# Optimization experiments

Measured on AMD Instinct MI355X. Metric: run time of the kernel, lower is better.

The kernel has to match this reference:

```python
import jax, jax.numpy as jnp
import numpy as np

H = 512          # hidden_size
HALF = 256       # hidden_size // 2 (RGCN feature dim)
NHEAD = 8
NLAYER = 12
NBLOCK = 2
NENT = 50000
NREL = 12
NBASES = 8
NEDGE = 500000
TXTD = 768       # raw text/image feature dim
BATCH, ELEN, SLEN = 32, 50, 128


def setup_inputs() -> dict:
    key = jax.random.key(0)
    ks = jax.random.split(key, 40)
    def p(i, shape, scale=0.02):
        return jax.random.normal(ks[i], shape, jnp.float32) * scale
    inp = {
        'entity_ids': jax.random.randint(ks[0], (BATCH, ELEN), 0, NENT),
        'token_embeds': jax.random.normal(ks[1], (BATCH, SLEN, H), jnp.float32),
        'edge_index': jax.random.randint(ks[2], (2, NEDGE), 0, NENT),
        'edge_type': jax.random.randint(ks[3], (NEDGE,), 0, NREL),
        'node_embeds': p(4, (NENT, HALF)),
        'rgcn_basis': p(5, (NBASES, HALF, HALF)),
        'rgcn_comp': p(6, (NREL, NBASES), 0.3),
        'rgcn_root': p(7, (HALF, HALF)),
        'rgcn_bias': p(8, (HALF,)),
        'kg_proj_w': p(9, (HALF, H)), 'kg_proj_b': p(10, (H,)),
        'text_proj_w': p(11, (TXTD, H)), 'text_proj_b': p(12, (H,)),
        'image_proj_w': p(13, (TXTD, H)), 'image_proj_b': p(14, (H,)),
        'cq_w': p(15, (H, H)), 'cq_b': p(16, (H,)),
        'kgk_w': p(17, (H, H)), 'kgk_b': p(18, (H,)),
        'imk_w': p(19, (H, H)), 'imk_b': p(20, (H,)),
        'txk_w': p(21, (H, H)), 'txk_b': p(22, (H,)),
        'pp1_w1': p(23, (H, HALF)), 'pp1_b1': p(24, (HALF,)),
        'pp1_w2': p(25, (HALF, H)), 'pp1_b2': p(26, (H,)),
        'pp2_w': p(27, (H, NLAYER * NBLOCK * H)), 'pp2_b': p(28, (NLAYER * NBLOCK * H,)),
        'text_embeds_init': p(29, (NENT, TXTD), 1.0),
        'image_embeds_init': p(30, (NENT, TXTD), 1.0),
    }
    return inp


def _rgcn(x, edge_index, edge_type, basis, comp, root, bias):
    # PyG RGCNConv with basis decomposition, aggr='mean', root weight + bias.
    # mean_{e: rel=r, dst=i}(x[src_e] @ W_r) == (mean_{e}(x[src_e])) @ W_r, so we
    # aggregate raw features per (dst, relation) segment then apply W_r once per node.
    N = x.shape[0]
    src, dst = edge_index[0], edge_index[1]
    seg = dst * NREL + edge_type                      # combined (node, relation) key
    msgs = x[src]                                     # [E, HALF] gather
    agg = jax.ops.segment_sum(msgs, seg, num_segments=N * NREL)
    cnt = jax.ops.segment_sum(jnp.ones((src.shape[0],), x.dtype), seg, num_segments=N * NREL)
    mean = (agg / jnp.maximum(cnt, 1.0)[:, None]).reshape(N, NREL, HALF)
    w_rel = jnp.einsum('rb,bio->rio', comp, basis)    # [R, HALF, HALF]
    out = jnp.einsum('nri,rio->no', mean, w_rel) + x @ root + bias
    return out


def reference(entity_ids, token_embeds, edge_index, edge_type, node_embeds,
              rgcn_basis, rgcn_comp, rgcn_root, rgcn_bias,
              kg_proj_w, kg_proj_b, text_proj_w, text_proj_b,
              image_proj_w, image_proj_b, cq_w, cq_b,
              kgk_w, kgk_b, imk_w, imk_b, txk_w, txk_b,
              pp1_w1, pp1_b1, pp1_w2, pp1_b2, pp2_w, pp2_b,
              text_embeds_init, image_embeds_init):
    kg_all = _rgcn(node_embeds, edge_index, edge_type, rgcn_basis, rgcn_comp, rgcn_root, rgcn_bias)
    kg_all = kg_all @ kg_proj_w + kg_proj_b           # [N, H]
    kg_feat = kg_all[entity_ids]                      # [B, L, H]
    text_feat = text_embeds_init[entity_ids] @ text_proj_w + text_proj_b
    image_feat = image_embeds_init[entity_ids] @ image_proj_w + image_proj_b
    # context-guided fusion
    q = (jnp.mean(token_embeds, axis=1) @ cq_w + cq_b)[:, None, :]   # [B, 1, H]
    kg_s = jnp.sum(q * (kg_feat @ kgk_w + kgk_b), -1, keepdims=True)
    img_s = jnp.sum(q * (image_feat @ imk_w + imk_b), -1, keepdims=True)
    txt_s = jnp.sum(q * (text_feat @ txk_w + txk_b), -1, keepdims=True)
    w = jax.nn.softmax(jnp.concatenate([kg_s, img_s, txt_s], axis=-1), axis=-1)
    fused = w[..., 0:1] * kg_feat + w[..., 1:2] * image_feat + w[..., 2:3] * text_feat
    # prompt expansion
    h = jax.nn.relu(fused @ pp1_w1 + pp1_b1) @ pp1_w2 + pp1_b2 + fused
    p = h @ pp2_w + pp2_b                             # [B, L, NLAYER*NBLOCK*H]
    B, L = entity_ids.shape
    p = p.reshape(B, L, NLAYER, NBLOCK, NHEAD, H // NHEAD)
    p = jnp.transpose(p, (2, 3, 0, 4, 1, 5))          # [layer, block, B, head, L, head_dim]
    loss_cl = jnp.float32(0.0)                        # output_entity=False path
    return p, loss_cl
```

## Files before the change

### kernel.cpp

```cpp
#include <hip/hip_runtime.h>

#define HDIM 512
#define HALF 256
#define NRELS 12
#define NBASES 8
#define NLAYERS 12
#define NBLOCKS 2
#define NHEADS 8
#define NENTS 50000
#define TXTD 768
#define BATCH 32
#define ELEN 50
#define SLEN 128
#define NPOS (BATCH * ELEN)
#define NSEG (NPOS * NRELS)
#define BCAP 64

typedef unsigned short u16;
typedef __attribute__((ext_vector_type(8))) __bf16 bf16x8;
typedef __attribute__((ext_vector_type(4))) float f32x4;

__device__ __forceinline__ u16 f2bf(float f) {
    unsigned int u = __float_as_uint(f);
    unsigned int r = (u + 0x7FFFu + ((u >> 16) & 1u)) >> 16;
    return (u16)r;
}
__device__ __forceinline__ float bf2f(u16 v) {
    return __uint_as_float(((unsigned int)v) << 16);
}

#define ASYNC_COPY16(g, l)                                                              \
    __builtin_amdgcn_global_load_lds((const __attribute__((address_space(1))) void*)(g), \
                                     (__attribute__((address_space(3))) unsigned int*)(l), 16, 0, 0)

__global__ void init_kernel(int* __restrict__ map, int* __restrict__ segcnt,
                            int* __restrict__ nuniq, float* __restrict__ zb,
                            const float* __restrict__ kgb, const float* __restrict__ imb,
                            const float* __restrict__ txb, u16* __restrict__ SW,
                            const float* __restrict__ rgcn_bias,
                            const float* __restrict__ kg_proj_w,
                            const float* __restrict__ kg_proj_b,
                            float* __restrict__ biasC, float* __restrict__ out_last) {
    int blk = blockIdx.x;
    int t = threadIdx.x;
    if (blk >= 128) {
        int n = (blk - 128) * 256 + t;
        float acc = kg_proj_b[n];
        for (int c = 0; c < HALF; ++c) acc += rgcn_bias[c] * kg_proj_w[(size_t)c * HDIM + n];
        biasC[n] = acc;
        return;
    }
    int tid = blk * 256 + t;
    const int nt = 128 * 256;
    int4 m4 = {-1, -1, -1, -1};
    for (int i = tid; i < NENTS / 4; i += nt) ((int4*)map)[i] = m4;
    int4 z4 = {0, 0, 0, 0};
    for (int i = tid; i < NSEG / 4; i += nt) ((int4*)segcnt)[i] = z4;
    for (int i = tid; i < 2304; i += nt) zb[i] = 0.f;
    if (tid < HDIM) {
        SW[(size_t)1536 * HDIM + tid] = f2bf(kgb[tid]);
        SW[(size_t)1537 * HDIM + tid] = f2bf(imb[tid]);
        SW[(size_t)1538 * HDIM + tid] = f2bf(txb[tid]);
    }
    if (tid == 0) { *nuniq = 0; *out_last = 0.f; }
}

__global__ void dedup_kernel(const int* __restrict__ eid, int* __restrict__ map,
                             int* __restrict__ uniq, int* __restrict__ nuniq) {
    int i = blockIdx.x * blockDim.x + threadIdx.x;
    if (i >= NPOS) return;
    int n = eid[i];
    int old = atomicCAS(&map[n], -1, -2);
    if (old == -1) {
        int idx = atomicAdd(nuniq, 1);
        uniq[idx] = n;
        __threadfence();
        map[n] = idx;
    }
}

struct PrepArgs {
    const float* src[12];
    u16* dst[12];
};

__global__ __launch_bounds__(256) void midprep_kernel(
    const float* __restrict__ tok, u16* __restrict__ TMEAN,
    const int* __restrict__ uniq, const int* __restrict__ nuniq,
    const float* __restrict__ txi, const float* __restrict__ imi,
    u16* __restrict__ TXIN, u16* __restrict__ IMIN,
    const int* __restrict__ ei, const int* __restrict__ et, const int* __restrict__ map,
    int* __restrict__ segcnt, int* __restrict__ bucket, int E, PrepArgs a) {
    int blk = blockIdx.x;
    int t = threadIdx.x;
    if (blk < 64) {
        int b = blk >> 1;
        int col = (blk & 1) * 256 + t;
        float s = 0.f;
        for (int si = 0; si < SLEN; ++si) s += tok[((size_t)b * SLEN + si) * HDIM + col];
        TMEAN[(size_t)b * HDIM + col] = f2bf(s * (1.0f / SLEN));
    } else if (blk < 352) {
        if (t >= TXTD / 4) return;
        int nu = *nuniq;
        for (int u = blk - 64; u < NPOS; u += 288) {
            if (u >= nu) {
                ushort4 z = {0, 0, 0, 0};
                ((ushort4*)(TXIN + (size_t)u * TXTD))[t] = z;
                ((ushort4*)(IMIN + (size_t)u * TXTD))[t] = z;
                continue;
            }
            int n = uniq[u];
            float4 v = ((const float4*)(txi + (size_t)n * TXTD))[t];
            ushort4 o;
            o.x = f2bf(v.x); o.y = f2bf(v.y); o.z = f2bf(v.z); o.w = f2bf(v.w);
            ((ushort4*)(TXIN + (size_t)u * TXTD))[t] = o;
            v = ((const float4*)(imi + (size_t)n * TXTD))[t];
            o.x = f2bf(v.x); o.y = f2bf(v.y); o.z = f2bf(v.z); o.w = f2bf(v.w);
            ((ushort4*)(IMIN + (size_t)u * TXTD))[t] = o;
        }
    } else if (blk < 864) {
        const int* __restrict__ dstA = ei + E;
        int gtid = (blk - 352) * 256 + t;
        int e0 = gtid * 4;
        if (e0 + 3 < E) {
            int4 d4 = *(const int4*)(dstA + e0);
            int4 t4 = *(const int4*)(et + e0);
            int cc0 = map[d4.x], cc1 = map[d4.y], cc2 = map[d4.z], cc3 = map[d4.w];
            if (cc0 >= 0) {
                int seg = cc0 * NRELS + t4.x;
                int p = atomicAdd(&segcnt[seg], 1);
                if (p < BCAP) bucket[seg * BCAP + p] = ei[e0];
            }
            if (cc1 >= 0) {
                int seg = cc1 * NRELS + t4.y;
                int p = atomicAdd(&segcnt[seg], 1);
                if (p < BCAP) bucket[seg * BCAP + p] = ei[e0 + 1];
            }
            if (cc2 >= 0) {
                int seg = cc2 * NRELS + t4.z;
                int p = atomicAdd(&segcnt[seg], 1);
                if (p < BCAP) bucket[seg * BCAP + p] = ei[e0 + 2];
            }
            if (cc3 >= 0) {
                int seg = cc3 * NRELS + t4.w;
                int p = atomicAdd(&segcnt[seg], 1);
                if (p < BCAP) bucket[seg * BCAP + p] = ei[e0 + 3];
            }
        } else {
            for (int e = e0; e < E; ++e) {
                int c = map[dstA[e]];
                if (c >= 0) {
                    int seg = c * NRELS + et[e];
                    int p = atomicAdd(&segcnt[seg], 1);
                    if (p < BCAP) bucket[seg * BCAP + p] = ei[e];
                }
            }
        }
    } else {
        constexpr int NN[7]  = {512, 512, 512, 256, 512, 12288, 512};
        constexpr int LDT[7] = {256, 768, 768, 512, 256, 512, 512};
        constexpr int BASE[13] = {0, 32, 128, 224, 256, 288, 1824,
                                  1888, 2400, 2464, 2720, 2976, 3232};
        __shared__ u16 tb[64][65];
        int bid = blk - 864;
        int op = 0;
        #pragma unroll
        for (int i = 1; i < 12; ++i)
            if (bid >= BASE[i]) op = i;
        int idx = bid - BASE[op];
        if (op < 7) {
            int Nv = 0, ldt = 0;
            #pragma unroll
            for (int i = 0; i < 7; ++i)
                if (op == i) { Nv = NN[i]; ldt = LDT[i]; }
            int ncols = Nv >> 6;
            int n0 = (idx % ncols) * 64, k0 = (idx / ncols) * 64;
            const float* W = a.src[op];
            u16* WT = a.dst[op];
            int lane = t & 63, wv = t >> 6;
            #pragma unroll
            for (int i2 = 0; i2 < 16; ++i2) {
                int r = wv * 16 + i2;
                tb[r][lane] = f2bf(W[(size_t)(k0 + r) * Nv + n0 + lane]);
            }
            __syncthreads();
            #pragma unroll
            for (int i2 = 0; i2 < 16; ++i2) {
                int rr = wv * 16 + i2;
                WT[(size_t)(n0 + rr) * ldt + k0 + lane] = tb[lane][rr];
            }
        } else {
            int e = idx * 1024 + t * 4;
            float4 v = *(const float4*)(a.src[op] + e);
            ushort4 o;
            o.x = f2bf(v.x); o.y = f2bf(v.y); o.z = f2bf(v.z); o.w = f2bf(v.w);
            *(ushort4*)(a.dst[op] + e) = o;
        }
    }
}

template <int BM, int BN, int WM, int WN, bool SCATTER>
__device__ __forceinline__ void gemm_body(const u16* __restrict__ A, const u16* __restrict__ BT,
                                          const float* __restrict__ bias,
                                          void* __restrict__ Cout, int M, int N, int K,
                                          int bx, int by, bool outbf) {
    constexpr int MF = WM / 16, NF = WN / 16;
    constexpr int NWC = BN / WN;
    __shared__ u16 ldsA[BM][64];
    __shared__ u16 ldsB[BN][64];
    const int tid = threadIdx.x;
    const int lane = tid & 63;
    const int wv = tid >> 6;
    const int m0 = by * BM;
    const int n0 = bx * BN;
    const int wr = wv / NWC, wc = wv % NWC;
    const int srow = lane >> 3;
    const int sslot = lane & 7;

    f32x4 acc[MF][NF];
    #pragma unroll
    for (int i = 0; i < MF; ++i)
        #pragma unroll
        for (int j = 0; j < NF; ++j)
            #pragma unroll
            for (int r = 0; r < 4; ++r) acc[i][j][r] = 0.f;

    for (int k0 = 0; k0 < K; k0 += 64) {
        #pragma unroll
        for (int i = 0; i < BM / 32; ++i) {
            int R = wv * (BM / 4) + i * 8 + srow;
            int gm = m0 + R;
            gm = gm < M ? gm : M - 1;
            int s = sslot ^ (R & 7);
            ASYNC_COPY16(A + (size_t)gm * K + k0 + s * 8, &ldsA[wv * (BM / 4) + i * 8][0]);
        }
        #pragma unroll
        for (int i = 0; i < BN / 32; ++i) {
            int R = wv * (BN / 4) + i * 8 + srow;
            int s = sslot ^ (R & 7);
            ASYNC_COPY16(BT + (size_t)(n0 + R) * K + k0 + s * 8, &ldsB[wv * (BN / 4) + i * 8][0]);
        }
        __syncthreads();
        #pragma unroll
        for (int ks = 0; ks < 2; ++ks) {
            bf16x8 af[MF], bf[NF];
            int kg = ks * 4 + (lane >> 4);
            int rl = lane & 15;
            #pragma unroll
            for (int i = 0; i < MF; ++i) {
                int row = wr * WM + i * 16 + rl;
                af[i] = *(const bf16x8*)&ldsA[row][(kg ^ (row & 7)) * 8];
            }
            #pragma unroll
            for (int j = 0; j < NF; ++j) {
                int row = wc * WN + j * 16 + rl;
                bf[j] = *(const bf16x8*)&ldsB[row][(kg ^ (row & 7)) * 8];
            }
            #pragma unroll
            for (int i = 0; i < MF; ++i)
                #pragma unroll
                for (int j = 0; j < NF; ++j)
                    acc[i][j] = __builtin_amdgcn_mfma_f32_16x16x32_bf16(af[i], bf[j], acc[i][j], 0, 0, 0);
        }
        __syncthreads();
    }

    const int rl = lane & 15, rg = lane >> 4;
    #pragma unroll
    for (int i = 0; i < MF; ++i) {
        #pragma unroll
        for (int j = 0; j < NF; ++j) {
            int col = n0 + wc * WN + j * 16 + rl;
            float bv = bias[col];
            #pragma unroll
            for (int r = 0; r < 4; ++r) {
                int row = m0 + wr * WM + i * 16 + rg * 4 + r;
                if (row >= M) continue;
                float x = acc[i][j][r] + bv;
                if (SCATTER) {
                    int layer = col >> 10, blk = (col >> 9) & 1, head = (col >> 6) & 7, hd = col & 63;
                    int bb = row / ELEN, ll = row - bb * ELEN;
                    size_t oi = (((((size_t)layer * NBLOCKS + blk) * BATCH + bb) * NHEADS + head) * ELEN + ll) * 64 + hd;
                    ((float*)Cout)[oi] = x;
                } else if (outbf) {
                    ((u16*)Cout)[(size_t)row * N + col] = f2bf(x);
                } else {
                    ((float*)Cout)[(size_t)row * N + col] = x;
                }
            }
        }
    }
}

struct BuildArgs {
    const int *segcnt, *bucket, *uniq, *nuniq;
    const float *comp, *x;
    u16* MBX;
    const u16 *TMEAN, *CQT;
    const float* cq_b;
    u16* QB;
    const u16 *KGT, *W1f;
    const float* ZB;
    u16* WC;
    const u16 *TXIN, *TXT, *IMIN, *IMT;
    const float *txb, *imb;
    u16 *TXU, *IMU;
};
__global__ __launch_bounds__(256) void build_kernel(BuildArgs a) {
    int blk = blockIdx.x;
    if (blk >= NPOS) {
        const u16 *A, *BT;
        const float* bias;
        u16* C;
        int M, N, K, bx, by;
        if (blk >= NPOS + 8 + 288 + 200) {
            int i = blk - (NPOS + 8 + 288 + 200);
            A = a.IMIN; BT = a.IMT; bias = a.imb; C = a.IMU;
            M = NPOS; N = HDIM; K = TXTD; bx = i % 8; by = i / 8;
        } else if (blk >= NPOS + 8 + 288) {
            int i = blk - (NPOS + 8 + 288);
            A = a.TXIN; BT = a.TXT; bias = a.txb; C = a.TXU;
            M = NPOS; N = HDIM; K = TXTD; bx = i % 8; by = i / 8;
        } else if (blk >= NPOS + 8) {
            int i = blk - (NPOS + 8);
            A = a.KGT; BT = a.W1f; bias = a.ZB; C = a.WC;
            M = HDIM; N = 2304; K = HALF; bx = i % 36; by = i / 36;
        } else {
            A = a.TMEAN; BT = a.CQT; bias = a.cq_b; C = a.QB;
            M = BATCH; N = HDIM; K = HDIM; bx = blk - NPOS; by = 0;
        }
        gemm_body<64, 64, 32, 32, false>(A, BT, bias, C, M, N, K, bx, by, true);
        return;
    }
    int u = blk;
    int i = threadIdx.x;
    __shared__ float sc[NRELS * NBASES];
    if (i < NRELS * NBASES) sc[i] = a.comp[i];
    __syncthreads();
    u16* row = a.MBX + (size_t)u * 2304;
    int nu = *a.nuniq;
    if (u >= nu) {
        for (int b = 0; b < NBASES + 1; ++b) row[b * HALF + i] = 0;
        return;
    }
    float mr[NRELS];
    #pragma unroll
    for (int r = 0; r < NRELS; ++r) {
        int seg = u * NRELS + r;
        int c = a.segcnt[seg];
        int n = min(c, BCAP);
        float acc = 0.f;
        for (int e = 0; e < n; ++e) {
            int s = a.bucket[seg * BCAP + e];
            acc += a.x[(size_t)s * HALF + i];
        }
        mr[r] = acc * (1.f / fmaxf((float)c, 1.f));
    }
    #pragma unroll
    for (int b = 0; b < NBASES; ++b) {
        float v = 0.f;
        #pragma unroll
        for (int r = 0; r < NRELS; ++r) v += sc[r * NBASES + b] * mr[r];
        row[b * HALF + i] = f2bf(v);
    }
    row[NBASES * HALF + i] = f2bf(a.x[(size_t)a.uniq[u] * HALF + i]);
}

struct ProjArgs {
    const u16 *MBX, *WC, *QB, *SW;
    const float *biasC, *ZB;
    u16* KGU;
    float* QP;
};
__global__ __launch_bounds__(256) void proj_kernel(ProjArgs a) {
    int b = blockIdx.x;
    if (b < 200) {
        gemm_body<64, 64, 32, 32, false>(a.MBX, a.WC, a.biasC, a.KGU,
                                         NPOS, HDIM, 2304, b % 8, b / 8, true);
    } else {
        gemm_body<64, 64, 32, 32, false>(a.QB, a.SW, a.ZB, a.QP,
                                         BATCH, 1600, HDIM, b - 200, 0, false);
    }
}

__global__ __launch_bounds__(256) void tail_kernel(
    const int* __restrict__ eid, const int* __restrict__ map,
    const u16* __restrict__ KGU, const u16* __restrict__ IMU, const u16* __restrict__ TXU,
    const float* __restrict__ qp,
    const u16* __restrict__ W1T, const float* __restrict__ pp1_b1,
    const u16* __restrict__ W2T, const float* __restrict__ pp1_b2,
    u16* __restrict__ Hh) {
    __shared__ u16 FUS[16][520];
    __shared__ u16 P1s[16][264];
    const int bm0 = blockIdx.x * 16;
    const int lane = threadIdx.x & 63;
    const int wv = threadIdx.x >> 6;

    for (int rr = wv; rr < 16; rr += 4) {
        int bl = bm0 + rr;
        int b = bl / ELEN;
        int u = map[eid[bl]];
        const u16* kg = KGU + (size_t)u * HDIM;
        const u16* im = IMU + (size_t)u * HDIM;
        const u16* tx = TXU + (size_t)u * HDIM;
        const float* qrow = qp + (size_t)b * 1600;
        float pkg = 0.f, pim = 0.f, ptx = 0.f;
        for (int e = lane; e < HDIM; e += 64) {
            pkg += bf2f(kg[e]) * qrow[e];
            pim += bf2f(im[e]) * qrow[512 + e];
            ptx += bf2f(tx[e]) * qrow[1024 + e];
        }
        #pragma unroll
        for (int off = 32; off; off >>= 1) {
            pkg += __shfl_down(pkg, off);
            pim += __shfl_down(pim, off);
            ptx += __shfl_down(ptx, off);
        }
        float w0, w1, w2;
        if (lane == 0) {
            float av = pkg + qrow[1536];
            float c1 = pim + qrow[1537];
            float c2 = ptx + qrow[1538];
            float mx = fmaxf(av, fmaxf(c1, c2));
            float ea = __expf(av - mx), eb = __expf(c1 - mx), ec = __expf(c2 - mx);
            float inv = 1.f / (ea + eb + ec);
            w0 = ea * inv; w1 = eb * inv; w2 = ec * inv;
        }
        w0 = __shfl(w0, 0); w1 = __shfl(w1, 0); w2 = __shfl(w2, 0);
        for (int e = lane; e < HDIM; e += 64) {
            float v = w0 * bf2f(kg[e]) + w1 * bf2f(im[e]) + w2 * bf2f(tx[e]);
            FUS[rr][e] = f2bf(v);
        }
    }
    __syncthreads();

    {
        const int rl = lane & 15;
        const int kgrp = lane >> 4;
        f32x4 acc[4];
        #pragma unroll
        for (int j = 0; j < 4; ++j)
            #pragma unroll
            for (int r = 0; r < 4; ++r) acc[j][r] = 0.f;
        for (int kk = 0; kk < 512; kk += 32) {
            int k8 = kk + kgrp * 8;
            bf16x8 af = *(const bf16x8*)&FUS[rl][k8];
            bf16x8 bf[4];
            #pragma unroll
            for (int j = 0; j < 4; ++j) {
                int n = wv * 64 + j * 16 + rl;
                bf[j] = *(const bf16x8*)&W1T[(size_t)n * 512 + k8];
            }
            #pragma unroll
            for (int j = 0; j < 4; ++j)
                acc[j] = __builtin_amdgcn_mfma_f32_16x16x32_bf16(af, bf[j], acc[j], 0, 0, 0);
        }
        const int rg = lane >> 4;
        #pragma unroll
        for (int j = 0; j < 4; ++j) {
            int col = wv * 64 + j * 16 + rl;
            float bv = pp1_b1[col];
            #pragma unroll
            for (int r = 0; r < 4; ++r) {
                int row = rg * 4 + r;
                P1s[row][col] = f2bf(fmaxf(acc[j][r] + bv, 0.f));
            }
        }
    }
    __syncthreads();

    {
        const int rl = lane & 15;
        const int kgrp = lane >> 4;
        f32x4 acc[8];
        #pragma unroll
        for (int j = 0; j < 8; ++j)
            #pragma unroll
            for (int r = 0; r < 4; ++r) acc[j][r] = 0.f;
        for (int kk = 0; kk < 256; kk += 32) {
            int k8 = kk + kgrp * 8;
            bf16x8 af = *(const bf16x8*)&P1s[rl][k8];
            bf16x8 bf[8];
            #pragma unroll
            for (int j = 0; j < 8; ++j) {
                int n = wv * 128 + j * 16 + rl;
                bf[j] = *(const bf16x8*)&W2T[(size_t)n * 256 + k8];
            }
            #pragma unroll
            for (int j = 0; j < 8; ++j)
                acc[j] = __builtin_amdgcn_mfma_f32_16x16x32_bf16(af, bf[j], acc[j], 0, 0, 0);
        }
        const int rg = lane >> 4;
        #pragma unroll
        for (int j = 0; j < 8; ++j) {
            int col = wv * 128 + j * 16 + rl;
            float bv = pp1_b2[col];
            #pragma unroll
            for (int r = 0; r < 4; ++r) {
                int row = rg * 4 + r;
                float v = acc[j][r] + bv + bf2f(FUS[row][col]);
                Hh[(size_t)(bm0 + row) * HDIM + col] = f2bf(v);
            }
        }
    }
}

__global__ __launch_bounds__(256)
void pp2_kernel(const u16* __restrict__ A, const u16* __restrict__ BT,
                const float* __restrict__ bias, void* __restrict__ Cout,
                int M, int N, int K) {
    gemm_body<128, 128, 64, 64, true>(A, BT, bias, Cout, M, N, K, blockIdx.x, blockIdx.y, false);
}

extern "C" void kernel_launch(void* const* d_in, const int* in_sizes, int n_in,
                              void* d_out, int out_size, void* d_ws, size_t ws_size,
                              hipStream_t stream) {
    const int* entity_ids = (const int*)d_in[0];
    const float* token_embeds = (const float*)d_in[1];
    const int* edge_index = (const int*)d_in[2];
    const int* edge_type = (const int*)d_in[3];
    const float* node_embeds = (const float*)d_in[4];
    const float* rgcn_basis = (const float*)d_in[5];
    const float* rgcn_comp = (const float*)d_in[6];
    const float* rgcn_root = (const float*)d_in[7];
    const float* rgcn_bias = (const float*)d_in[8];
    const float* kg_proj_w = (const float*)d_in[9];
    const float* kg_proj_b = (const float*)d_in[10];
    const float* text_proj_w = (const float*)d_in[11];
    const float* text_proj_b = (const float*)d_in[12];
    const float* image_proj_w = (const float*)d_in[13];
    const float* image_proj_b = (const float*)d_in[14];
    const float* cq_w = (const float*)d_in[15];
    const float* cq_b = (const float*)d_in[16];
    const float* kgk_w = (const float*)d_in[17];
    const float* imk_w = (const float*)d_in[19];
    const float* txk_w = (const float*)d_in[21];
    const float* pp1_w1 = (const float*)d_in[23];
    const float* pp1_b1 = (const float*)d_in[24];
    const float* pp1_w2 = (const float*)d_in[25];
    const float* pp1_b2 = (const float*)d_in[26];
    const float* pp2_w = (const float*)d_in[27];
    const float* pp2_b = (const float*)d_in[28];
    const float* text_init = (const float*)d_in[29];
    const float* image_init = (const float*)d_in[30];

    const int E = in_sizes[3];

    size_t off = 0;
    auto alloc = [&](size_t bytes) { size_t o = off; off += (bytes + 255) & ~(size_t)255; return o; };
    char* ws = (char*)d_ws;
    size_t map_o  = alloc((size_t)NENTS * 4);
    size_t nun_o  = alloc(4);
    size_t unq_o  = alloc((size_t)NPOS * 4);
    size_t scnt_o = alloc((size_t)NSEG * 4);
    size_t bkt_o  = alloc((size_t)NSEG * BCAP * 4);
    size_t mbx_o  = alloc((size_t)NPOS * 2304 * 2);
    size_t w1f_o  = alloc((size_t)2304 * HALF * 2);
    size_t wc_o   = alloc((size_t)HDIM * 2304 * 2);
    size_t bc_o   = alloc((size_t)HDIM * 4);
    size_t kgt_o  = alloc((size_t)HDIM * HALF * 2);
    size_t kgu_o  = alloc((size_t)NPOS * HDIM * 2);
    size_t txin_o = alloc((size_t)NPOS * TXTD * 2);
    size_t imin_o = alloc((size_t)NPOS * TXTD * 2);
    size_t txt_o  = alloc((size_t)HDIM * TXTD * 2);
    size_t imt_o  = alloc((size_t)HDIM * TXTD * 2);
    size_t txu_o  = alloc((size_t)NPOS * HDIM * 2);
    size_t imu_o  = alloc((size_t)NPOS * HDIM * 2);
    size_t tm_o   = alloc((size_t)BATCH * HDIM * 2);
    size_t qb_o   = alloc((size_t)BATCH * HDIM * 2);
    size_t cqt_o  = alloc((size_t)HDIM * HDIM * 2);
    size_t sw_o   = alloc((size_t)1600 * HDIM * 2);
    size_t qp_o   = alloc((size_t)BATCH * 1600 * 4);
    size_t zb_o   = alloc((size_t)2304 * 4);
    size_t w1t_o  = alloc((size_t)HALF * HDIM * 2);
    size_t w2t_o  = alloc((size_t)HDIM * HALF * 2);
    size_t h_o    = alloc((size_t)NPOS * HDIM * 2);
    size_t pp2t_o = alloc((size_t)12288 * HDIM * 2);
    if (off > ws_size) return;

    int* map = (int*)(ws + map_o);
    int* nuniq = (int*)(ws + nun_o);
    int* uniq = (int*)(ws + unq_o);
    int* segcnt = (int*)(ws + scnt_o);
    int* bucket = (int*)(ws + bkt_o);
    u16* MBX = (u16*)(ws + mbx_o);
    u16* W1f = (u16*)(ws + w1f_o);
    u16* WC  = (u16*)(ws + wc_o);
    float* biasC = (float*)(ws + bc_o);
    u16* KGT = (u16*)(ws + kgt_o);
    u16* KGU = (u16*)(ws + kgu_o);
    u16* TXIN = (u16*)(ws + txin_o);
    u16* IMIN = (u16*)(ws + imin_o);
    u16* TXT = (u16*)(ws + txt_o);
    u16* IMT = (u16*)(ws + imt_o);
    u16* TXU = (u16*)(ws + txu_o);
    u16* IMU = (u16*)(ws + imu_o);
    u16* TMEAN = (u16*)(ws + tm_o);
    u16* QB  = (u16*)(ws + qb_o);
    u16* CQT = (u16*)(ws + cqt_o);
    u16* SW  = (u16*)(ws + sw_o);
    float* QP  = (float*)(ws + qp_o);
    float* ZB  = (float*)(ws + zb_o);
    u16* W1T = (u16*)(ws + w1t_o);
    u16* W2T = (u16*)(ws + w2t_o);
    u16* Hh  = (u16*)(ws + h_o);
    u16* PP2T = (u16*)(ws + pp2t_o);
    float* OUT = (float*)d_out;

    init_kernel<<<130, 256, 0, stream>>>(map, segcnt, nuniq, ZB,
                                         (const float*)d_in[18], (const float*)d_in[20],
                                         (const float*)d_in[22], SW,
                                         rgcn_bias, kg_proj_w, kg_proj_b, biasC,
                                         OUT + (out_size - 1));
    dedup_kernel<<<(NPOS + 255) / 256, 256, 0, stream>>>(entity_ids, map, uniq, nuniq);
    PrepArgs pa;
    pa.src[0] = kg_proj_w;    pa.dst[0] = KGT;
    pa.src[1] = text_proj_w;  pa.dst[1] = TXT;
    pa.src[2] = image_proj_w; pa.dst[2] = IMT;
    pa.src[3] = pp1_w1;       pa.dst[3] = W1T;
    pa.src[4] = pp1_w2;       pa.dst[4] = W2T;
    pa.src[5] = pp2_w;        pa.dst[5] = PP2T;
    pa.src[6] = cq_w;         pa.dst[6] = CQT;
    pa.src[7] = rgcn_basis;   pa.dst[7] = W1f;
    pa.src[8] = rgcn_root;    pa.dst[8] = W1f + (size_t)2048 * HALF;
    pa.src[9] = kgk_w;        pa.dst[9] = SW;
    pa.src[10] = imk_w;       pa.dst[10] = SW + (size_t)HDIM * HDIM;
    pa.src[11] = txk_w;       pa.dst[11] = SW + (size_t)2 * HDIM * HDIM;
    midprep_kernel<<<4096, 256, 0, stream>>>(token_embeds, TMEAN,
                                             uniq, nuniq, text_init, image_init, TXIN, IMIN,
                                             edge_index, edge_type, map, segcnt, bucket, E, pa);
    BuildArgs ba;
    ba.segcnt = segcnt; ba.bucket = bucket; ba.uniq = uniq; ba.nuniq = nuniq;
    ba.comp = rgcn_comp; ba.x = node_embeds; ba.MBX = MBX;
    ba.TMEAN = TMEAN; ba.CQT = CQT; ba.cq_b = cq_b; ba.QB = QB;
    ba.KGT = KGT; ba.W1f = W1f; ba.ZB = ZB; ba.WC = WC;
    ba.TXIN = TXIN; ba.TXT = TXT; ba.IMIN = IMIN; ba.IMT = IMT;
    ba.txb = text_proj_b; ba.imb = image_proj_b; ba.TXU = TXU; ba.IMU = IMU;
    build_kernel<<<NPOS + 8 + 288 + 400, 256, 0, stream>>>(ba);
    ProjArgs pr;
    pr.MBX = MBX; pr.WC = WC; pr.biasC = biasC; pr.KGU = KGU;
    pr.QB = QB; pr.SW = SW; pr.ZB = ZB; pr.QP = QP;
    proj_kernel<<<225, 256, 0, stream>>>(pr);
    tail_kernel<<<NPOS / 16, 256, 0, stream>>>(entity_ids, map, KGU, IMU, TXU, QP,
                                               W1T, pp1_b1, W2T, pp1_b2, Hh);
    pp2_kernel<<<dim3(12288 / 128, (NPOS + 127) / 128), 256, 0, stream>>>(
        Hh, PP2T, pp2_b, OUT, NPOS, 12288, HDIM);
}
```

Measured before the change: 152.3 us.

## Replace pp2 GEMM with dedicated 128x256 tile, 8-wave kernel with fused transpose store

The final large projection GEMM no longer uses the generic gemm_body. It gets its own kernel with a 128x256 output tile, 512 threads (8 waves in a 2x4 grid), XOR-swizzled LDS staging via async copies, and a 4x4 MFMA accumulator block per wave. The epilogue adds the bias and writes straight into the permuted [layer, block, batch, head, L, head_dim] layout. The wider tile is meant to improve A-operand reuse and MFMA density. In exchange the kernel has no double buffering across k-steps, uses higher register pressure, and launches half as many blocks.

```diff
diff --git a/kernel.cpp b/kernel.cpp
--- a/kernel.cpp
+++ b/kernel.cpp
@@ -505,11 +505,89 @@
     }
 }
 
-__global__ __launch_bounds__(256)
+__global__ __launch_bounds__(512)
 void pp2_kernel(const u16* __restrict__ A, const u16* __restrict__ BT,
-                const float* __restrict__ bias, void* __restrict__ Cout,
+                const float* __restrict__ bias, float* __restrict__ Cout,
                 int M, int N, int K) {
-    gemm_body<128, 128, 64, 64, true>(A, BT, bias, Cout, M, N, K, blockIdx.x, blockIdx.y, false);
+    __shared__ u16 ldsA[128][64];
+    __shared__ u16 ldsB[256][64];
+    const int tid = threadIdx.x;
+    const int lane = tid & 63;
+    const int wv = tid >> 6;
+    const int m0 = blockIdx.y * 128;
+    const int n0 = blockIdx.x * 256;
+    const int wr = wv >> 2;
+    const int wc = wv & 3;
+    const int srow = lane >> 3;
+    const int sslot = lane & 7;
+
+    f32x4 acc[4][4];
+    #pragma unroll
+    for (int i = 0; i < 4; ++i)
+        #pragma unroll
+        for (int j = 0; j < 4; ++j)
+            #pragma unroll
+            for (int r = 0; r < 4; ++r) acc[i][j][r] = 0.f;
+
+    for (int k0 = 0; k0 < K; k0 += 64) {
+        #pragma unroll
+        for (int i = 0; i < 2; ++i) {
+            int R = wv * 16 + i * 8 + srow;
+            int gm = m0 + R;
+            gm = gm < M ? gm : M - 1;
+            int s = sslot ^ (R & 7);
+            ASYNC_COPY16(A + (size_t)gm * K + k0 + s * 8, &ldsA[wv * 16 + i * 8][0]);
+        }
+        #pragma unroll
+        for (int i = 0; i < 4; ++i) {
+            int R = wv * 32 + i * 8 + srow;
+            int s = sslot ^ (R & 7);
+            ASYNC_COPY16(BT + (size_t)(n0 + R) * K + k0 + s * 8, &ldsB[wv * 32 + i * 8][0]);
+        }
+        __syncthreads();
+        #pragma unroll
+        for (int ks = 0; ks < 2; ++ks) {
+            bf16x8 af[4], bf[4];
+            int kg = ks * 4 + (lane >> 4);
+            int rl = lane & 15;
+            #pragma unroll
+            for (int i = 0; i < 4; ++i) {
+                int row = wr * 64 + i * 16 + rl;
+                af[i] = *(const bf16x8*)&ldsA[row][(kg ^ (row & 7)) * 8];
+            }
+            #pragma unroll
+            for (int j = 0; j < 4; ++j) {
+                int row = wc * 64 + j * 16 + rl;
+                bf[j] = *(const bf16x8*)&ldsB[row][(kg ^ (row & 7)) * 8];
+            }
+            #pragma unroll
+            for (int i = 0; i < 4; ++i)
+                #pragma unroll
+                for (int j = 0; j < 4; ++j)
+                    acc[i][j] = __builtin_amdgcn_mfma_f32_16x16x32_bf16(af[i], bf[j], acc[i][j], 0, 0, 0);
+        }
+        __syncthreads();
+    }
+
+    const int rl = lane & 15, rg = lane >> 4;
+    #pragma unroll
+    for (int i = 0; i < 4; ++i) {
+        #pragma unroll
+        for (int j = 0; j < 4; ++j) {
+            int col = n0 + wc * 64 + j * 16 + rl;
+            float bv = bias[col];
+            #pragma unroll
+            for (int r = 0; r < 4; ++r) {
+                int row = m0 + wr * 64 + i * 16 + rg * 4 + r;
+                if (row >= M) continue;
+                float x = acc[i][j][r] + bv;
+                int layer = col >> 10, blk = (col >> 9) & 1, head = (col >> 6) & 7, hd = col & 63;
+                int bb = row / ELEN, ll = row - bb * ELEN;
+                size_t oi = (((((size_t)layer * NBLOCKS + blk) * BATCH + bb) * NHEADS + head) * ELEN + ll) * 64 + hd;
+                Cout[oi] = x;
+            }
+        }
+    }
 }
 
 extern "C" void kernel_launch(void* const* d_in, const int* in_sizes, int n_in,
@@ -643,6 +721,6 @@
     proj_kernel<<<225, 256, 0, stream>>>(pr);
     tail_kernel<<<NPOS / 16, 256, 0, stream>>>(entity_ids, map, KGU, IMU, TXU, QP,
                                                W1T, pp1_b1, W2T, pp1_b2, Hh);
-    pp2_kernel<<<dim3(12288 / 128, (NPOS + 127) / 128), 256, 0, stream>>>(
+    pp2_kernel<<<dim3(12288 / 256, (NPOS + 127) / 128), 512, 0, stream>>>(
         Hh, PP2T, pp2_b, OUT, NPOS, 12288, HDIM);
 }
```

Result: no change. 154.1 us (+1.2%).
